# Optimization experiments

Measured on AMD Instinct MI355X. Metric: run time of the kernel, lower is better.

Reference implementation:

```python
import jax, jax.numpy as jnp
import numpy as np

E, D, H = 8, 512, 2048   # n_experts, d_model, d_ff (Mlp default hidden = 4*dim)
B, N = 8, 512            # batch, seq_len -> T = 4096 tokens


def setup_inputs() -> dict:
    key = jax.random.key(0)
    ks = jax.random.split(key, 4)
    def init(k, shape, fan_in):
        return jax.random.normal(k, shape, jnp.float32) * (1.0 / np.sqrt(fan_in))
    return {
        "x": jax.random.normal(ks[0], (B, N, D), jnp.float32),
        "Wr": init(ks[1], (D, E), D),          # router (switch) weight
        "br": jnp.zeros((E,), jnp.float32),
        "W1": init(ks[2], (E, D, H), D),       # per-expert fc1
        "b1": jnp.zeros((E, H), jnp.float32),
        "W2": init(ks[3], (E, H, D), H),       # per-expert fc2
        "b2": jnp.zeros((E, D), jnp.float32),
    }


def reference(x, Wr, br, W1, b1, W2, b2):
    b, n, d = x.shape
    xt = x.reshape(-1, d)                                  # [T, D]
    # Router runs in float32 (torch.autocast disabled in original).
    route_prob = jax.nn.softmax(xt.astype(jnp.float32) @ Wr + br, axis=-1)  # [T, E]
    routes = jnp.argmax(route_prob, axis=-1)               # [T] top-1 expert
    p_max = jnp.max(route_prob, axis=-1)                   # [T]

    # drop_tokens=False: every token goes through exactly its argmax expert.
    # Scan over experts; mask-combine avoids dynamic per-expert batch sizes
    # while only materializing one [T, H] intermediate at a time.
    def expert_step(acc, inp):
        w1, bb1, w2, bb2, e = inp
        h = jax.nn.gelu(xt @ w1 + bb1, approximate=False)  # [T, H], exact GELU as nn.GELU
        y = h @ w2 + bb2                                   # [T, D]
        return acc + y * (routes == e)[:, None].astype(y.dtype), None

    out, _ = jax.lax.scan(expert_step, jnp.zeros_like(xt),
                          (W1, b1, W2, b2, jnp.arange(E)))
    # is_scale_prob=False branch: multiply by p / p.detach() (==1 in fwd,
    # but routes gradient through the router probabilities).
    out = out * (p_max / jax.lax.stop_gradient(p_max))[:, None]
    return out.reshape(b, n, d)
```

## Files before the change

### kernel.cpp

```cpp
#include <hip/hip_runtime.h>
#include <math.h>

#define TOK 4096
#define DM  512
#define HF  2048
#define NE  8
#define PD 544
#define PH 2080

typedef __bf16 bf16x8 __attribute__((ext_vector_type(8)));
typedef float  floatx16 __attribute__((ext_vector_type(16)));

__device__ __forceinline__ unsigned short f2b(float f) {
    union { float f; unsigned u; } v; v.f = f;
    return (unsigned short)((v.u + 0x7fffu + ((v.u >> 16) & 1u)) >> 16);
}

__device__ __forceinline__ void load_lds16(const void* g, void* l) {
    __builtin_amdgcn_global_load_lds(
        (__attribute__((address_space(1))) unsigned int*)g,
        (__attribute__((address_space(3))) unsigned int*)l, 16, 0, 0);
}

template <int NTHR>
__device__ __forceinline__ void transpose_tile(unsigned short (*tile)[68],
                                               const float* __restrict__ src,
                                               unsigned short* __restrict__ dst,
                                               int K, int N, int dstS,
                                               int k0, int n0) {
#pragma unroll
    for (int i = 0; i < 1024 / NTHR; i++) {
        int it = threadIdx.x + i * NTHR;
        int r = it >> 4, tc = it & 15;
        const float4 v = *(const float4*)(src + (size_t)(k0 + r) * N + n0 + tc * 4);
        tile[r][tc * 4 + 0] = f2b(v.x);
        tile[r][tc * 4 + 1] = f2b(v.y);
        tile[r][tc * 4 + 2] = f2b(v.z);
        tile[r][tc * 4 + 3] = f2b(v.w);
    }
    __syncthreads();
#pragma unroll
    for (int i = 0; i < 1024 / NTHR; i++) {
        int it = threadIdx.x + i * NTHR;
        int nrow = it >> 4, tc = it & 15;
        ushort4 o;
        o.x = tile[tc * 4 + 0][nrow];
        o.y = tile[tc * 4 + 1][nrow];
        o.z = tile[tc * 4 + 2][nrow];
        o.w = tile[tc * 4 + 3][nrow];
        *(ushort4*)(dst + (size_t)(n0 + nrow) * dstS + k0 + tc * 4) = o;
    }
}

__global__ __launch_bounds__(256)
void k_router_trW1(const float* __restrict__ x, const float* __restrict__ Wr,
                   const float* __restrict__ br, const float* __restrict__ W1,
                   int* __restrict__ routes, unsigned short* __restrict__ xb,
                   unsigned short* __restrict__ W1t) {
    if (blockIdx.x >= TOK / 4) {
        __shared__ unsigned short tl[64][68];
        int bt = blockIdx.x - TOK / 4;
        int e = bt & 7, tile = bt >> 3;
        transpose_tile<256>(tl, W1 + (size_t)e * DM * HF, W1t + (size_t)e * HF * PD,
                            DM, HF, PD, (tile >> 5) * 64, (tile & 31) * 64);
        return;
    }
    int t = blockIdx.x * 4 + (threadIdx.x >> 6);
    int lane = threadIdx.x & 63;
    const float4* xr = (const float4*)(x + (size_t)t * DM);
    float4 v0 = xr[lane * 2 + 0];
    float4 v1 = xr[lane * 2 + 1];
    float xv[8] = {v0.x, v0.y, v0.z, v0.w, v1.x, v1.y, v1.z, v1.w};

    union { unsigned short u[8]; int4 q; } pk;
#pragma unroll
    for (int k = 0; k < 8; k++) pk.u[k] = f2b(xv[k]);
    *(int4*)(xb + (size_t)t * PD + lane * 8) = pk.q;

    float acc[NE];
#pragma unroll
    for (int e = 0; e < NE; e++) acc[e] = 0.f;
#pragma unroll
    for (int k = 0; k < 8; k++) {
        const float* w = Wr + (size_t)(lane * 8 + k) * NE;
        float4 wa = *(const float4*)(w);
        float4 wb = *(const float4*)(w + 4);
        acc[0] += xv[k] * wa.x; acc[1] += xv[k] * wa.y;
        acc[2] += xv[k] * wa.z; acc[3] += xv[k] * wa.w;
        acc[4] += xv[k] * wb.x; acc[5] += xv[k] * wb.y;
        acc[6] += xv[k] * wb.z; acc[7] += xv[k] * wb.w;
    }
#pragma unroll
    for (int off = 32; off > 0; off >>= 1)
#pragma unroll
        for (int e = 0; e < NE; e++) acc[e] += __shfl_down(acc[e], off, 64);
    if (lane == 0) {
        int best = 0; float bv = acc[0] + br[0];
#pragma unroll
        for (int e = 1; e < NE; e++) {
            float v = acc[e] + br[e];
            if (v > bv) { bv = v; best = e; }
        }
        routes[t] = best;
    }
}

__global__ __launch_bounds__(1024)
void k_organize(const int* __restrict__ routes, int* __restrict__ offsets,
                int* __restrict__ perm) {
    __shared__ int wcnt[16][NE], wbase[16][NE], off[NE + 1], tot[NE];
    int tid = threadIdx.x, lane = tid & 63, w = tid >> 6;
    int4 r4 = *(const int4*)&routes[tid * 4];
    int e_[4] = {r4.x, r4.y, r4.z, r4.w};
    unsigned long long below = (1ull << lane) - 1ull;
    int rank[4];
#pragma unroll
    for (int e = 0; e < NE; e++) {
        int c = 0;
#pragma unroll
        for (int j = 0; j < 4; j++) {
            unsigned long long m = __ballot(e_[j] == e);
            if (e_[j] == e) rank[j] = c + __popcll(m & below);
            c += __popcll(m);
        }
        if (lane == 0) wcnt[w][e] = c;
    }
    __syncthreads();
    if (tid < NE) {
        int s = 0;
#pragma unroll
        for (int ww = 0; ww < 16; ww++) { wbase[ww][tid] = s; s += wcnt[ww][tid]; }
        tot[tid] = s;
    }
    __syncthreads();
    if (tid == 0) {
        int s = 0;
#pragma unroll
        for (int e = 0; e < NE; e++) { off[e] = s; s += tot[e]; }
        off[NE] = s;
    }
    __syncthreads();
#pragma unroll
    for (int j = 0; j < 4; j++) {
        int e = e_[j];
        perm[off[e] + wbase[w][e] + rank[j]] = tid * 4 + j;
    }
    if (tid < NE + 1) offsets[tid] = off[tid];
}

template <int KD, int KP, int ND, bool FC1, int KSPLIT, int XT, int YT>
__global__ __launch_bounds__(256)
void k_gemm(const unsigned short* __restrict__ A,
            const unsigned short* __restrict__ Bt,
            const float* __restrict__ bias,
            unsigned short* __restrict__ hg,
            float* __restrict__ pbuf,
            const int* __restrict__ offsets,
            const int* __restrict__ perm,
            const float* __restrict__ W2s,
            unsigned short* __restrict__ W2d) {
    __shared__ unsigned short smem[12288];

    const int id = blockIdx.x;
    if constexpr (FC1) {
        if (id >= NE * XT * YT) {
            int bt = id - NE * XT * YT;
            int e2 = bt & 7, tl = bt >> 3;
            transpose_tile<256>((unsigned short(*)[68])smem,
                                W2s + (size_t)e2 * HF * DM, W2d + (size_t)e2 * DM * PH,
                                HF, DM, PH, (tl >> 3) * 64, (tl & 7) * 64);
            return;
        }
    }
    const int e  = id & 7;
    int t = id >> 3;
    const int ks = t % KSPLIT; t /= KSPLIT;
    const int bx = t % XT;
    const int by = t / XT;

    const int seg0 = offsets[e];
    const int cnt  = offsets[e + 1] - seg0;
    const int m0 = by * 64;
    if (m0 >= cnt) return;
    const int n0 = bx * 128;

    const unsigned short* Bexp = Bt + (size_t)e * ND * KP;

    const int tid  = threadIdx.x;
    const int lane = tid & 63;
    const int wave = tid >> 6;
    const int wm = (wave >> 1) * 32;
    const int wn = (wave & 1) * 64;

    const unsigned short* aSrc;
    const unsigned short* bSrc[2];
    const int foA = tid * 16;
    {
        int row = foA >> 6;
        int c   = ((foA >> 4) & 3) ^ ((row >> 1) & 3);
        if constexpr (FC1) {
            int idx = seg0 + m0 + row;
            if (idx > TOK - 1) idx = TOK - 1;
            aSrc = A + (size_t)perm[idx] * KP + c * 8;
        } else {
            aSrc = A + (size_t)(seg0 + m0 + row) * KP + c * 8;
        }
    }
    int foB[2];
#pragma unroll
    for (int r = 0; r < 2; r++) {
        int fo  = tid * 16 + r * 4096;
        int row = fo >> 6;
        int c   = ((fo >> 4) & 3) ^ ((row >> 1) & 3);
        foB[r] = fo;
        bSrc[r] = Bexp + (size_t)(n0 + row) * KP + c * 8;
    }
    auto stage = [&](int k0, int buf) {
        char* ab = (char*)(smem + buf * 6144);
        char* bb = (char*)(smem + buf * 6144 + 2048);
        load_lds16(aSrc + k0, ab + foA);
#pragma unroll
        for (int r = 0; r < 2; r++) load_lds16(bSrc[r] + k0, bb + foB[r]);
    };

    const int fr = lane & 31;
    const int hi = lane >> 5;
    const int q  = (lane >> 1) & 3;
    const int sw[2] = { ((0 + hi) ^ q) * 8, ((2 + hi) ^ q) * 8 };
    const int aBase = (wm + fr) * 32;
    const int bBase = (wn + fr) * 32;

    floatx16 acc[2];
#pragma unroll
    for (int j = 0; j < 2; j++)
#pragma unroll
        for (int r = 0; r < 16; r++) acc[j][r] = 0.f;

    const int kBase = ks * (KD / KSPLIT);
    const int kEnd  = kBase + (KD / KSPLIT);
    stage(kBase, 0);
    int cur = 0;
    for (int k0 = kBase; k0 < kEnd; k0 += 32) {
        __syncthreads();
        if (k0 + 32 < kEnd) stage(k0 + 32, cur ^ 1);
        const unsigned short* Ab = smem + cur * 6144;
        const unsigned short* Bb = smem + cur * 6144 + 2048;
#pragma unroll
        for (int kk = 0; kk < 2; kk++) {
            bf16x8 af = *(const bf16x8*)&Ab[aBase + sw[kk]];
            bf16x8 bf[2];
#pragma unroll
            for (int j = 0; j < 2; j++)
                bf[j] = *(const bf16x8*)&Bb[bBase + j * 1024 + sw[kk]];
#pragma unroll
            for (int j = 0; j < 2; j++)
                acc[j] = __builtin_amdgcn_mfma_f32_32x32x16_bf16(af, bf[j], acc[j], 0, 0, 0);
        }
        cur ^= 1;
    }

    const int rbase = 4 * hi;
#pragma unroll
    for (int j = 0; j < 2; j++) {
        int col = n0 + wn + j * 32 + fr;
        float bv = FC1 ? bias[(size_t)e * ND + col] : 0.f;
#pragma unroll
        for (int r = 0; r < 16; r++) {
            int grow = m0 + wm + rbase + (r & 3) + 8 * (r >> 2);
            if (grow < cnt) {
                float v = acc[j][r] + bv;
                if constexpr (FC1) {
                    v = 0.5f * v * (1.0f + erff(v * 0.70710678118654752f));
                    hg[(size_t)(seg0 + grow) * PH + col] = f2b(v);
                } else {
                    pbuf[((size_t)ks * TOK + seg0 + grow) * ND + col] = v;
                }
            }
        }
    }
}

__global__ __launch_bounds__(128)
void k_reduce(const float* __restrict__ pbuf, const int* __restrict__ perm,
              const int* __restrict__ offsets, const float* __restrict__ b2,
              float* __restrict__ out) {
    int g = blockIdx.x;
    int tok = perm[g];
    int e = 0;
#pragma unroll
    for (int i = 1; i < NE; i++) e += (g >= offsets[i]);
    int c = threadIdx.x * 4;
    float4 o = *(const float4*)&b2[(size_t)e * DM + c];
#pragma unroll
    for (int ks = 0; ks < 4; ks++) {
        float4 a = *(const float4*)&pbuf[((size_t)ks * TOK + g) * DM + c];
        o.x += a.x; o.y += a.y; o.z += a.z; o.w += a.w;
    }
    *(float4*)&out[(size_t)tok * DM + c] = o;
}

extern "C" void kernel_launch(void* const* d_in, const int* in_sizes, int n_in,
                              void* d_out, int out_size, void* d_ws, size_t ws_size,
                              hipStream_t stream) {
    const float* x  = (const float*)d_in[0];
    const float* Wr = (const float*)d_in[1];
    const float* br = (const float*)d_in[2];
    const float* W1 = (const float*)d_in[3];
    const float* b1 = (const float*)d_in[4];
    const float* W2 = (const float*)d_in[5];
    const float* b2 = (const float*)d_in[6];
    float* out = (float*)d_out;

    char* ws = (char*)d_ws;
    int* routes  = (int*)ws;
    int* perm    = routes + TOK;
    int* offsets = perm + TOK;
    unsigned short* xb  = (unsigned short*)(ws + 65536);
    unsigned short* hg  = xb + (size_t)TOK * PD;
    unsigned short* W1t = hg + (size_t)TOK * PH;
    unsigned short* W2t = W1t + (size_t)NE * HF * PD;
    float* pbuf = (float*)(W2t + (size_t)NE * DM * PH);

    k_router_trW1<<<TOK / 4 + 2048, 256, 0, stream>>>(x, Wr, br, W1, routes, xb, W1t);
    k_organize<<<1, 1024, 0, stream>>>(routes, offsets, perm);
    k_gemm<DM, PD, HF, true, 1, 16, 16><<<NE * 256 + 2048, 256, 0, stream>>>(
        xb, W1t, b1, hg, nullptr, offsets, perm, W2, W2t);
    k_gemm<HF, PH, DM, false, 4, 4, 16><<<NE * 256, 256, 0, stream>>>(
        hg, W2t, nullptr, nullptr, pbuf, offsets, perm, nullptr, nullptr);
    k_reduce<<<TOK, 128, 0, stream>>>(pbuf, perm, offsets, b2, out);
}
```

Before: 83.59 us.

## Interleave W2 transpose with FC1 GEMM blocks and halve FC2 K-split

Reorders the FC1 launch so W2 transpose blocks are interleaved with GEMM blocks per expert instead of appended at the end, letting the transpose overlap with GEMM work. Reduces the FC2 split-K factor from 4 to 2, halving the partial-sum buffer traffic and reduce work at the cost of fewer, longer FC2 blocks. Uses nontemporal stores and loads for the partial buffer and output.

```diff
diff --git a/kernel.cpp b/kernel.cpp
--- a/kernel.cpp
+++ b/kernel.cpp
@@ -10,6 +10,7 @@
 
 typedef __bf16 bf16x8 __attribute__((ext_vector_type(8)));
 typedef float  floatx16 __attribute__((ext_vector_type(16)));
+typedef float  f4n __attribute__((ext_vector_type(4)));
 
 __device__ __forceinline__ unsigned short f2b(float f) {
     union { float f; unsigned u; } v; v.f = f;
@@ -162,21 +163,26 @@
     __shared__ unsigned short smem[12288];
 
     const int id = blockIdx.x;
+    int e, bx, by, ks;
     if constexpr (FC1) {
-        if (id >= NE * XT * YT) {
-            int bt = id - NE * XT * YT;
-            int e2 = bt & 7, tl = bt >> 3;
+        int g = id >> 4;
+        e = id & 7;
+        if ((id >> 3) & 1) {
             transpose_tile<256>((unsigned short(*)[68])smem,
-                                W2s + (size_t)e2 * HF * DM, W2d + (size_t)e2 * DM * PH,
-                                HF, DM, PH, (tl >> 3) * 64, (tl & 7) * 64);
+                                W2s + (size_t)e * HF * DM, W2d + (size_t)e * DM * PH,
+                                HF, DM, PH, (g >> 3) * 64, (g & 7) * 64);
             return;
         }
-    }
-    const int e  = id & 7;
-    int t = id >> 3;
-    const int ks = t % KSPLIT; t /= KSPLIT;
-    const int bx = t % XT;
-    const int by = t / XT;
+        bx = g & (XT - 1);
+        by = g >> 4;
+        ks = 0;
+    } else {
+        e = id & 7;
+        int t = id >> 3;
+        ks = t % KSPLIT; t /= KSPLIT;
+        bx = t % XT;
+        by = t / XT;
+    }
 
     const int seg0 = offsets[e];
     const int cnt  = offsets[e + 1] - seg0;
@@ -273,7 +279,8 @@
                     v = 0.5f * v * (1.0f + erff(v * 0.70710678118654752f));
                     hg[(size_t)(seg0 + grow) * PH + col] = f2b(v);
                 } else {
-                    pbuf[((size_t)ks * TOK + seg0 + grow) * ND + col] = v;
+                    __builtin_nontemporal_store(
+                        v, &pbuf[((size_t)ks * TOK + seg0 + grow) * ND + col]);
                 }
             }
         }
@@ -290,13 +297,14 @@
 #pragma unroll
     for (int i = 1; i < NE; i++) e += (g >= offsets[i]);
     int c = threadIdx.x * 4;
-    float4 o = *(const float4*)&b2[(size_t)e * DM + c];
-#pragma unroll
-    for (int ks = 0; ks < 4; ks++) {
-        float4 a = *(const float4*)&pbuf[((size_t)ks * TOK + g) * DM + c];
-        o.x += a.x; o.y += a.y; o.z += a.z; o.w += a.w;
-    }
-    *(float4*)&out[(size_t)tok * DM + c] = o;
+    f4n o = *(const f4n*)&b2[(size_t)e * DM + c];
+#pragma unroll
+    for (int ks = 0; ks < 2; ks++) {
+        const f4n* p = (const f4n*)&pbuf[((size_t)ks * TOK + g) * DM + c];
+        f4n a = __builtin_nontemporal_load(p);
+        o += a;
+    }
+    __builtin_nontemporal_store(o, (f4n*)&out[(size_t)tok * DM + c]);
 }
 
 extern "C" void kernel_launch(void* const* d_in, const int* in_sizes, int n_in,
@@ -323,9 +331,9 @@
 
     k_router_trW1<<<TOK / 4 + 2048, 256, 0, stream>>>(x, Wr, br, W1, routes, xb, W1t);
     k_organize<<<1, 1024, 0, stream>>>(routes, offsets, perm);
-    k_gemm<DM, PD, HF, true, 1, 16, 16><<<NE * 256 + 2048, 256, 0, stream>>>(
+    k_gemm<DM, PD, HF, true, 1, 16, 16><<<4096, 256, 0, stream>>>(
         xb, W1t, b1, hg, nullptr, offsets, perm, W2, W2t);
-    k_gemm<HF, PH, DM, false, 4, 4, 16><<<NE * 256, 256, 0, stream>>>(
+    k_gemm<HF, PH, DM, false, 2, 4, 16><<<NE * 128, 256, 0, stream>>>(
         hg, W2t, nullptr, nullptr, pbuf, offsets, perm, nullptr, nullptr);
     k_reduce<<<TOK, 128, 0, stream>>>(pbuf, perm, offsets, b2, out);
 }
```

New measurement: 96.70 us. 15.7% more time.
